# Kernel optimization log

Measured on AMD Instinct MI355X. Metric: run time of the kernel, lower is better.

## Reference

```python
import jax, jax.numpy as jnp
import numpy as np

TOKENS = 32768
D_MODEL = 4096
N_EXPERTS = 64
BALANCE_LOSS_WEIGHT = 0.1


def setup_inputs() -> dict:
    key = jax.random.key(0)
    kx, kw1, kw2, kn = jax.random.split(key, 4)
    x = jax.random.normal(kx, (TOKENS, D_MODEL), dtype=jnp.float32)
    # torch nn.Linear weight layout: [out_features, in_features]
    w1 = jax.random.normal(kw1, (N_EXPERTS, D_MODEL), dtype=jnp.float32) / np.sqrt(D_MODEL)
    w2 = jax.random.normal(kw2, (N_EXPERTS, N_EXPERTS), dtype=jnp.float32) / np.sqrt(N_EXPERTS)
    # fixed Gumbel noise sample: g = -log(-log(u)), matching gumbel_rsample
    u = jax.random.uniform(kn, (TOKENS, N_EXPERTS), dtype=jnp.float32, minval=1e-8, maxval=1.0)
    noise = -jnp.log(-jnp.log(u))
    return {"x": x, "w1": w1, "w2": w2, "noise": noise}


def reference(x, w1, w2, noise):
    # MLP gate: Linear(d->E, no bias) -> tanh -> Linear(E->E, no bias)
    h = jnp.tanh(x @ w1.T)                       # [T, E]
    logits = h @ w2.T                             # [T, E]
    scores = jax.nn.softmax(logits, axis=1)       # [T, E]
    logits_w_noise = logits + noise               # gumbel-perturbed logits
    top1_indices = jnp.argmax(logits_w_noise, axis=1)   # [T] int
    top1_scores = jnp.max(logits_w_noise, axis=1)       # [T]
    # balance loss
    importance_mean = scores.mean(axis=0)                        # [E]
    load = jnp.bincount(top1_indices, length=N_EXPERTS)          # [E] int
    load_mean = load.astype(scores.dtype) / x.shape[0]           # [E]
    balance_loss = (N_EXPERTS * jnp.sum(importance_mean * load_mean)
                    * BALANCE_LOSS_WEIGHT)
    return (top1_indices, top1_scores, balance_loss, load_mean, importance_mean)
```

## Files before the change

kernel.cpp:

```cpp
#include <hip/hip_runtime.h>
#include <math.h>

#define TOKENS 32768
#define DM 4096
#define NE 64
#define BALW 0.1f

#define TG 64
#define GBLOCKS (TOKENS / TG)

typedef __attribute__((ext_vector_type(8))) short short8;
typedef __attribute__((ext_vector_type(4))) float f32x4;

typedef unsigned short us;

__device__ inline us bf16r(float f) {
  const unsigned u = __float_as_uint(f);
  return (us)((u + 0x7FFFu + ((u >> 16) & 1u)) >> 16);
}
__device__ inline float bf16f(us s) {
  return __uint_as_float(((unsigned)s) << 16);
}
__device__ inline void split8(const float4 v0, const float4 v1, short8& H,
                              short8& M, short8& L) {
  float v[8] = {v0.x, v0.y, v0.z, v0.w, v1.x, v1.y, v1.z, v1.w};
#pragma unroll
  for (int j = 0; j < 8; ++j) {
    const us hs = bf16r(v[j]);
    const float r1 = v[j] - bf16f(hs);
    const us ms = bf16r(r1);
    const float r2 = r1 - bf16f(ms);
    const us ls = bf16r(r2);
    H[j] = (short)hs; M[j] = (short)ms; L[j] = (short)ls;
  }
}

__device__ inline void split8t(const float4 v0, const float4 v1, short8& H,
                               short8& M, short8& L) {
  unsigned u[8], um[8], ul[8];
  const float v[8] = {v0.x, v0.y, v0.z, v0.w, v1.x, v1.y, v1.z, v1.w};
#pragma unroll
  for (int j = 0; j < 8; ++j) {
    u[j] = __float_as_uint(v[j]);
    const float r1 = v[j] - __uint_as_float(u[j] & 0xFFFF0000u);
    um[j] = __float_as_uint(r1);
    const float r2 = r1 - __uint_as_float(um[j] & 0xFFFF0000u);
    ul[j] = __float_as_uint(r2);
  }
  union Cvt { unsigned u4[4]; short8 s8; } h, m, l;
#pragma unroll
  for (int d = 0; d < 4; ++d) {
    h.u4[d] = __builtin_amdgcn_perm(u[2 * d + 1], u[2 * d], 0x07060302u);
    m.u4[d] = __builtin_amdgcn_perm(um[2 * d + 1], um[2 * d], 0x07060302u);
    l.u4[d] = __builtin_amdgcn_perm(ul[2 * d + 1], ul[2 * d], 0x07060302u);
  }
  H = h.s8; M = m.s8; L = l.s8;
}

#define MFMA(a, b, c) __builtin_amdgcn_mfma_f32_16x16x32_bf16(a, b, c, 0, 0, 0)

__global__ void prep_w1_kernel(const float* __restrict__ w1,
                               us* __restrict__ bws) {
  const int kc = blockIdx.x;
  const int tid = threadIdx.x;
  const int ns = tid >> 6;
  const int l = tid & 63;
  const int r = l & 15, g = l >> 4;
  const int n = 16 * ns + r;
  const int kb = 32 * kc + 8 * g;
  const float* src = &w1[(size_t)n * DM + kb];
  const float4 v0 = *reinterpret_cast<const float4*>(src);
  const float4 v1 = *reinterpret_cast<const float4*>(src + 4);
  short8 H, M, L;
  split8(v0, v1, H, M, L);
  us* dst = bws + ((size_t)(kc * 4 + ns) * 3) * 512 + l * 8;
  *reinterpret_cast<short8*>(dst) = H;
  *reinterpret_cast<short8*>(dst + 512) = M;
  *reinterpret_cast<short8*>(dst + 1024) = L;
}

#define TMM 128

template <int SK>
__global__ __launch_bounds__(256, 2) void gemm_mfma_kernel(
    const float* __restrict__ x, const us* __restrict__ bws,
    float* __restrict__ hp) {
  constexpr int KS = DM / SK;
  constexpr int NIT = KS / 32;
  const int tid = threadIdx.x;
  const int kz = blockIdx.x % SK;
  const int mb = blockIdx.x / SK;
  const int w = tid >> 6;
  const int l = tid & 63;
  const int r = l & 15, g = l >> 4;
  const int row0 = mb * TMM + w * 32;
  const int kb0 = kz * KS;

  f32x4 acc[2][4];
#pragma unroll
  for (int i = 0; i < 2; ++i)
#pragma unroll
    for (int j = 0; j < 4; ++j) acc[i][j] = (f32x4)(0.f);

  const float* xA0 = &x[(size_t)(row0 + r) * DM + kb0 + 8 * g];
  const float* xA1 = xA0 + (size_t)16 * DM;
  const us* bb = bws + (size_t)(kb0 / 32) * 12 * 512 + l * 8;

  float4 a00 = *reinterpret_cast<const float4*>(xA0);
  float4 a01 = *reinterpret_cast<const float4*>(xA0 + 4);
  float4 a10 = *reinterpret_cast<const float4*>(xA1);
  float4 a11 = *reinterpret_cast<const float4*>(xA1 + 4);
  short8 bf[4][3];
#pragma unroll
  for (int ns = 0; ns < 4; ++ns)
#pragma unroll
    for (int p = 0; p < 3; ++p)
      bf[ns][p] = *reinterpret_cast<const short8*>(bb + (ns * 3 + p) * 512);

  for (int it = 0; it < NIT; ++it) {
    const int itn = (it + 1 < NIT) ? it + 1 : it;
    const us* btn = bb + (size_t)itn * 12 * 512;
    const int ko = itn * 32;
    const float4 n00 = *reinterpret_cast<const float4*>(xA0 + ko);
    const float4 n01 = *reinterpret_cast<const float4*>(xA0 + ko + 4);
    const float4 n10 = *reinterpret_cast<const float4*>(xA1 + ko);
    const float4 n11 = *reinterpret_cast<const float4*>(xA1 + ko + 4);

    short8 ah0, am0, al0, ah1, am1, al1;
    split8t(a00, a01, ah0, am0, al0);
    split8t(a10, a11, ah1, am1, al1);

#define PROW(AH0, AH1, P)                                                \
  do {                                                                   \
    _Pragma("unroll") for (int ns = 0; ns < 4; ++ns) {                   \
      acc[0][ns] = MFMA(AH0, bf[ns][P], acc[0][ns]);                     \
      acc[1][ns] = MFMA(AH1, bf[ns][P], acc[1][ns]);                     \
    }                                                                    \
  } while (0)
#define RELOAD(P)                                                        \
  do {                                                                   \
    _Pragma("unroll") for (int ns = 0; ns < 4; ++ns) bf[ns][P] =         \
        *reinterpret_cast<const short8*>(btn + (ns * 3 + (P)) * 512);    \
  } while (0)

    PROW(ah0, ah1, 0);
    PROW(am0, am1, 0);
    PROW(al0, al1, 0);
    RELOAD(0);
    PROW(ah0, ah1, 1);
    PROW(am0, am1, 1);
    RELOAD(1);
    PROW(ah0, ah1, 2);
    RELOAD(2);
#undef PROW
#undef RELOAD

    a00 = n00; a01 = n01; a10 = n10; a11 = n11;
  }

  float* dst = hp + (size_t)kz * TOKENS * NE;
#pragma unroll
  for (int ms = 0; ms < 2; ++ms)
#pragma unroll
    for (int ns = 0; ns < 4; ++ns)
#pragma unroll
      for (int q = 0; q < 4; ++q)
        dst[(size_t)(row0 + 16 * ms + 4 * g + q) * NE + 16 * ns + r] =
            acc[ms][ns][q];
}

#define TM 128
#define BK 32
#define LDSA 132
#define LDSB 68

template <int SK>
__global__ __launch_bounds__(256, 4) void gemm_fp32_kernel(
    const float* __restrict__ x, const float* __restrict__ w1,
    float* __restrict__ hp) {
  constexpr int KS = DM / SK;
  __shared__ float As[BK * LDSA];
  __shared__ float Ws[BK * LDSB];
  const int tid = threadIdx.x;
  const int kz = blockIdx.x % SK;
  const int mb = blockIdx.x / SK;
  const int row0 = mb * TM;
  const int kbase = kz * KS;
  const int m0 = (tid >> 3) * 4;
  const int n0 = (tid & 7) * 8;
  const int rS = tid >> 2;
  const int kS = (tid & 3) * 4;

  float acc[4][8];
#pragma unroll
  for (int i = 0; i < 4; ++i)
#pragma unroll
    for (int j = 0; j < 8; ++j) acc[i][j] = 0.f;

  float4 ra[4], rw[2];
  const float* xp = &x[(size_t)(row0 + rS) * DM + kS];
  const float* wp = &w1[(size_t)rS * DM + kS];

#define LOAD_TILE(KC)                                                   \
  do {                                                                  \
    ra[0] = *reinterpret_cast<const float4*>(xp + (KC));                \
    ra[1] = *reinterpret_cast<const float4*>(xp + (KC) + 16);           \
    ra[2] = *reinterpret_cast<const float4*>(xp + (size_t)64 * DM + (KC));\
    ra[3] = *reinterpret_cast<const float4*>(xp + (size_t)64 * DM + (KC) + 16);\
    rw[0] = *reinterpret_cast<const float4*>(wp + (KC));                \
    rw[1] = *reinterpret_cast<const float4*>(wp + (KC) + 16);           \
  } while (0)

#define ST4(arr, stride, krow, col, v)                                  \
  do {                                                                  \
    arr[((krow) + 0) * (stride) + (col)] = (v).x;                       \
    arr[((krow) + 1) * (stride) + (col)] = (v).y;                       \
    arr[((krow) + 2) * (stride) + (col)] = (v).z;                       \
    arr[((krow) + 3) * (stride) + (col)] = (v).w;                       \
  } while (0)

#define STORE_TILE()                                                    \
  do {                                                                  \
    ST4(As, LDSA, kS, rS, ra[0]);                                       \
    ST4(As, LDSA, kS + 16, rS, ra[1]);                                  \
    ST4(As, LDSA, kS, rS + 64, ra[2]);                                  \
    ST4(As, LDSA, kS + 16, rS + 64, ra[3]);                             \
    ST4(Ws, LDSB, kS, rS, rw[0]);                                       \
    ST4(Ws, LDSB, kS + 16, rS, rw[1]);                                  \
  } while (0)

  LOAD_TILE(kbase);

  for (int kc = kbase; kc < kbase + KS; kc += BK) {
    __syncthreads();
    STORE_TILE();
    __syncthreads();
    if (kc + BK < kbase + KS) LOAD_TILE(kc + BK);
#pragma unroll 8
    for (int k = 0; k < BK; ++k) {
      const float4 a0 = *reinterpret_cast<const float4*>(&As[k * LDSA + m0]);
      const float4 b0 = *reinterpret_cast<const float4*>(&Ws[k * LDSB + n0]);
      const float4 b1 =
          *reinterpret_cast<const float4*>(&Ws[k * LDSB + n0 + 4]);
      const float a[4] = {a0.x, a0.y, a0.z, a0.w};
      const float b[8] = {b0.x, b0.y, b0.z, b0.w, b1.x, b1.y, b1.z, b1.w};
#pragma unroll
      for (int i = 0; i < 4; ++i)
#pragma unroll
        for (int j = 0; j < 8; ++j) acc[i][j] = fmaf(a[i], b[j], acc[i][j]);
    }
  }
#undef LOAD_TILE
#undef ST4
#undef STORE_TILE

  float* dst = hp + (size_t)kz * TOKENS * NE;
#pragma unroll
  for (int i = 0; i < 4; ++i) {
    const size_t o = (size_t)(row0 + m0 + i) * NE;
    *reinterpret_cast<float4*>(&dst[o + n0]) =
        make_float4(acc[i][0], acc[i][1], acc[i][2], acc[i][3]);
    *reinterpret_cast<float4*>(&dst[o + n0 + 4]) =
        make_float4(acc[i][4], acc[i][5], acc[i][6], acc[i][7]);
  }
}

template <int SK>
__global__ __launch_bounds__(256) void gate_kernel(
    const float* __restrict__ hp, const float* __restrict__ w2,
    const float* __restrict__ noise, float* __restrict__ out_idx,
    float* __restrict__ out_score, float* __restrict__ imp_part,
    float* __restrict__ load_part) {
  __shared__ float hs[TG * 65];
  __shared__ float w2s[NE * 65];
  __shared__ float ls[TG * 66];
  __shared__ float csum[2 * NE];
  __shared__ int hist[NE];
  const int tid = threadIdx.x;
  const int t0 = blockIdx.x * TG;
  if (tid < NE) hist[tid] = 0;

#pragma unroll
  for (int it = 0; it < 4; ++it) {
    const int f = tid + 256 * it;
    const int c = f & 15;
    const int t = f >> 4;
    const size_t g = (size_t)(t0 + t) * NE + c * 4;
    float4 p = *reinterpret_cast<const float4*>(&hp[g]);
#pragma unroll
    for (int s = 1; s < SK; ++s) {
      const float4 q =
          *reinterpret_cast<const float4*>(&hp[(size_t)s * TOKENS * NE + g]);
      p.x += q.x; p.y += q.y; p.z += q.z; p.w += q.w;
    }
    float* d = &hs[t * 65 + c * 4];
    d[0] = tanhf(p.x);
    d[1] = tanhf(p.y);
    d[2] = tanhf(p.z);
    d[3] = tanhf(p.w);
  }
#pragma unroll
  for (int it = 0; it < 4; ++it) {
    const int f = tid + 256 * it;
    const int c = f & 15;
    const int rr = f >> 4;
    const float4 v =
        *reinterpret_cast<const float4*>(&w2[(size_t)rr * NE + c * 4]);
    float* d = &w2s[rr * 65 + c * 4];
    d[0] = v.x; d[1] = v.y; d[2] = v.z; d[3] = v.w;
  }
  __syncthreads();

  {
    const int m0 = (tid >> 4) * 4;
    const int n0 = (tid & 15) * 4;
    float acc[4][4];
#pragma unroll
    for (int i = 0; i < 4; ++i)
#pragma unroll
      for (int j = 0; j < 4; ++j) acc[i][j] = 0.f;
#pragma unroll 8
    for (int k = 0; k < NE; ++k) {
      float a[4], b[4];
#pragma unroll
      for (int i = 0; i < 4; ++i) a[i] = hs[(m0 + i) * 65 + k];
#pragma unroll
      for (int j = 0; j < 4; ++j) b[j] = w2s[(n0 + j) * 65 + k];
#pragma unroll
      for (int i = 0; i < 4; ++i)
#pragma unroll
        for (int j = 0; j < 4; ++j) acc[i][j] = fmaf(a[i], b[j], acc[i][j]);
    }
#pragma unroll
    for (int i = 0; i < 4; ++i)
#pragma unroll
      for (int j = 0; j < 4; ++j) ls[(m0 + i) * 66 + n0 + j] = acc[i][j];
  }
  __syncthreads();

  if (tid < TG) {
    const int t = tid;
    float mx = -INFINITY, best = -INFINITY;
    int bi = 0;
    for (int e = 0; e < NE; ++e) {
      const float lv = ls[t * 66 + e];
      mx = fmaxf(mx, lv);
      const float gg = lv + noise[(size_t)(t0 + t) * NE + e];
      if (gg > best) { best = gg; bi = e; }
    }
    float s = 0.f;
    for (int e = 0; e < NE; ++e) {
      const float ex = expf(ls[t * 66 + e] - mx);
      s += ex;
      ls[t * 66 + e] = ex;
    }
    const float inv = 1.f / s;
    for (int e = 0; e < NE; ++e) ls[t * 66 + e] *= inv;
    out_idx[t0 + t] = (float)bi;
    out_score[t0 + t] = best;
    atomicAdd(&hist[bi], 1);
  }
  __syncthreads();

  if (tid < 128) {
    const int e = tid & 63;
    const int half = tid >> 6;
    float s = 0.f;
    for (int rr = half * 32; rr < half * 32 + 32; ++rr) s += ls[rr * 66 + e];
    csum[half * NE + e] = s;
  }
  __syncthreads();
  if (tid < NE) {
    imp_part[(size_t)blockIdx.x * NE + tid] = csum[tid] + csum[NE + tid];
    load_part[(size_t)blockIdx.x * NE + tid] = (float)hist[tid];
  }
}

__global__ void finalize_kernel(const float* __restrict__ imp_part,
                                const float* __restrict__ load_part,
                                float* __restrict__ out) {
  const int e = threadIdx.x;
  float imp = 0.f, ld = 0.f;
  for (int b = 0; b < GBLOCKS; ++b) {
    imp += imp_part[(size_t)b * NE + e];
    ld += load_part[(size_t)b * NE + e];
  }
  const float imp_mean = imp / (float)TOKENS;
  const float load_mean = ld / (float)TOKENS;
  out[2 * TOKENS + 1 + e] = load_mean;
  out[2 * TOKENS + 1 + NE + e] = imp_mean;
  float prod = imp_mean * load_mean;
#pragma unroll
  for (int off = 32; off > 0; off >>= 1) prod += __shfl_down(prod, off);
  if (e == 0) out[2 * TOKENS] = (float)NE * prod * BALW;
}

extern "C" void kernel_launch(void* const* d_in, const int* in_sizes, int n_in,
                              void* d_out, int out_size, void* d_ws,
                              size_t ws_size, hipStream_t stream) {
  const float* x = (const float*)d_in[0];
  const float* w1 = (const float*)d_in[1];
  const float* w2 = (const float*)d_in[2];
  const float* noise = (const float*)d_in[3];
  float* out = (float*)d_out;

  const size_t bws_shorts = (size_t)128 * 4 * 3 * 512;
  const size_t part_elems = (size_t)2 * GBLOCKS * NE;
  const size_t need_mfma = bws_shorts * sizeof(us) +
                           ((size_t)2 * TOKENS * NE + part_elems) *
                               sizeof(float);
  const size_t need_fp32 =
      ((size_t)2 * TOKENS * NE + part_elems) * sizeof(float);

  if (ws_size == 0 || ws_size >= need_mfma) {
    us* bws = (us*)d_ws;
    float* hp = (float*)(bws + bws_shorts);
    float* imp_part = hp + (size_t)2 * TOKENS * NE;
    float* load_part = imp_part + (size_t)GBLOCKS * NE;
    hipLaunchKernelGGL(prep_w1_kernel, dim3(128), dim3(256), 0, stream, w1,
                       bws);
    hipLaunchKernelGGL((gemm_mfma_kernel<2>), dim3((TOKENS / TMM) * 2),
                       dim3(256), 0, stream, x, bws, hp);
    hipLaunchKernelGGL((gate_kernel<2>), dim3(GBLOCKS), dim3(256), 0, stream,
                       hp, w2, noise, out, out + TOKENS, imp_part, load_part);
    hipLaunchKernelGGL(finalize_kernel, dim3(1), dim3(64), 0, stream, imp_part,
                       load_part, out);
  } else if (ws_size >= need_fp32) {
    float* hp = (float*)d_ws;
    float* imp_part = hp + (size_t)2 * TOKENS * NE;
    float* load_part = imp_part + (size_t)GBLOCKS * NE;
    hipLaunchKernelGGL((gemm_fp32_kernel<2>), dim3((TOKENS / TM) * 2),
                       dim3(256), 0, stream, x, w1, hp);
    hipLaunchKernelGGL((gate_kernel<2>), dim3(GBLOCKS), dim3(256), 0, stream,
                       hp, w2, noise, out, out + TOKENS, imp_part, load_part);
    hipLaunchKernelGGL(finalize_kernel, dim3(1), dim3(64), 0, stream, imp_part,
                       load_part, out);
  }
}
```

Before: 202.3 us.

## Stage x tiles through LDS with coalesced loads; parallelize finalize reduction

The MFMA GEMM now loads 128x128 chunks of x with fully coalesced row-contiguous float4 loads into registers and writes them to shared memory. The next chunk is prefetched while the current one is consumed from LDS by the MFMA waves. Before, each lane read 32-byte pieces straight from global memory with a strided pattern. The finalize kernel now uses 1024 threads, splitting the per-block partial reduction into 16 segments combined through shared memory instead of one 64-thread serial loop. The cost is extra LDS traffic, two barriers per chunk, and much higher register use for the 16 staged float4s.

After: 313.6 us. 55.0% more time.

```diff
diff --git a/kernel.cpp b/kernel.cpp
--- a/kernel.cpp
+++ b/kernel.cpp
@@ -79,21 +79,24 @@
   *reinterpret_cast<short8*>(dst + 1024) = L;
 }
 
-#define TMM 128
+#define TMB 128
+#define KO 128
 
 template <int SK>
 __global__ __launch_bounds__(256, 2) void gemm_mfma_kernel(
     const float* __restrict__ x, const us* __restrict__ bws,
     float* __restrict__ hp) {
   constexpr int KS = DM / SK;
-  constexpr int NIT = KS / 32;
+  constexpr int NOUT = KS / KO;
+  constexpr int NCH = KS / 32;
+  __shared__ float As[TMB * 132];
   const int tid = threadIdx.x;
   const int kz = blockIdx.x % SK;
   const int mb = blockIdx.x / SK;
   const int w = tid >> 6;
   const int l = tid & 63;
   const int r = l & 15, g = l >> 4;
-  const int row0 = mb * TMM + w * 32;
+  const int row0 = mb * TMB;
   const int kb0 = kz * KS;
 
   f32x4 acc[2][4];
@@ -102,14 +105,15 @@
 #pragma unroll
     for (int j = 0; j < 4; ++j) acc[i][j] = (f32x4)(0.f);
 
-  const float* xA0 = &x[(size_t)(row0 + r) * DM + kb0 + 8 * g];
-  const float* xA1 = xA0 + (size_t)16 * DM;
+  const float* xstage =
+      &x[(size_t)(row0 + (tid >> 5)) * DM + kb0 + (tid & 31) * 4];
+  const int lds_w = (8 * 0 + (tid >> 5)) * 132 + (tid & 31) * 4;
+  float4 sa[16];
+#pragma unroll
+  for (int q = 0; q < 16; ++q)
+    sa[q] = *reinterpret_cast<const float4*>(xstage + (size_t)(8 * q) * DM);
+
   const us* bb = bws + (size_t)(kb0 / 32) * 12 * 512 + l * 8;
-
-  float4 a00 = *reinterpret_cast<const float4*>(xA0);
-  float4 a01 = *reinterpret_cast<const float4*>(xA0 + 4);
-  float4 a10 = *reinterpret_cast<const float4*>(xA1);
-  float4 a11 = *reinterpret_cast<const float4*>(xA1 + 4);
   short8 bf[4][3];
 #pragma unroll
   for (int ns = 0; ns < 4; ++ns)
@@ -117,20 +121,41 @@
     for (int p = 0; p < 3; ++p)
       bf[ns][p] = *reinterpret_cast<const short8*>(bb + (ns * 3 + p) * 512);
 
-  for (int it = 0; it < NIT; ++it) {
-    const int itn = (it + 1 < NIT) ? it + 1 : it;
-    const us* btn = bb + (size_t)itn * 12 * 512;
-    const int ko = itn * 32;
-    const float4 n00 = *reinterpret_cast<const float4*>(xA0 + ko);
-    const float4 n01 = *reinterpret_cast<const float4*>(xA0 + ko + 4);
-    const float4 n10 = *reinterpret_cast<const float4*>(xA1 + ko);
-    const float4 n11 = *reinterpret_cast<const float4*>(xA1 + ko + 4);
-
-    short8 ah0, am0, al0, ah1, am1, al1;
-    split8t(a00, a01, ah0, am0, al0);
-    split8t(a10, a11, ah1, am1, al1);
-
-#define PROW(AH0, AH1, P)                                                \
+  const int rbase = 32 * w + r;
+
+  for (int o = 0; o < NOUT; ++o) {
+    __syncthreads();
+#pragma unroll
+    for (int q = 0; q < 16; ++q)
+      *reinterpret_cast<float4*>(&As[lds_w + q * 8 * 132]) = sa[q];
+    __syncthreads();
+    if (o + 1 < NOUT) {
+#pragma unroll
+      for (int q = 0; q < 16; ++q)
+        sa[q] = *reinterpret_cast<const float4*>(
+            xstage + (size_t)(8 * q) * DM + (o + 1) * KO);
+    }
+
+#pragma unroll
+    for (int c = 0; c < 4; ++c) {
+      const int ic = o * 4 + c;
+      const int icn = (ic + 1 < NCH) ? ic + 1 : ic;
+      const us* btn = bb + (size_t)icn * 12 * 512;
+      const int ca = 32 * c + 8 * g;
+      const float4 a00 =
+          *reinterpret_cast<const float4*>(&As[rbase * 132 + ca]);
+      const float4 a01 =
+          *reinterpret_cast<const float4*>(&As[rbase * 132 + ca + 4]);
+      const float4 a10 =
+          *reinterpret_cast<const float4*>(&As[(rbase + 16) * 132 + ca]);
+      const float4 a11 =
+          *reinterpret_cast<const float4*>(&As[(rbase + 16) * 132 + ca + 4]);
+
+      short8 ah0, am0, al0, ah1, am1, al1;
+      split8t(a00, a01, ah0, am0, al0);
+      split8t(a10, a11, ah1, am1, al1);
+
+#define PROW2(AH0, AH1, P)                                               \
   do {                                                                   \
     _Pragma("unroll") for (int ns = 0; ns < 4; ++ns) {                   \
       acc[0][ns] = MFMA(AH0, bf[ns][P], acc[0][ns]);                     \
@@ -143,30 +168,29 @@
         *reinterpret_cast<const short8*>(btn + (ns * 3 + (P)) * 512);    \
   } while (0)
 
-    PROW(ah0, ah1, 0);
-    PROW(am0, am1, 0);
-    PROW(al0, al1, 0);
-    RELOAD(0);
-    PROW(ah0, ah1, 1);
-    PROW(am0, am1, 1);
-    RELOAD(1);
-    PROW(ah0, ah1, 2);
-    RELOAD(2);
-#undef PROW
+      PROW2(ah0, ah1, 0);
+      PROW2(am0, am1, 0);
+      PROW2(al0, al1, 0);
+      RELOAD(0);
+      PROW2(ah0, ah1, 1);
+      PROW2(am0, am1, 1);
+      RELOAD(1);
+      PROW2(ah0, ah1, 2);
+      RELOAD(2);
+#undef PROW2
 #undef RELOAD
-
-    a00 = n00; a01 = n01; a10 = n10; a11 = n11;
+    }
   }
 
   float* dst = hp + (size_t)kz * TOKENS * NE;
 #pragma unroll
-  for (int ms = 0; ms < 2; ++ms)
+  for (int rg = 0; rg < 2; ++rg)
 #pragma unroll
     for (int ns = 0; ns < 4; ++ns)
 #pragma unroll
       for (int q = 0; q < 4; ++q)
-        dst[(size_t)(row0 + 16 * ms + 4 * g + q) * NE + 16 * ns + r] =
-            acc[ms][ns][q];
+        dst[(size_t)(row0 + 32 * w + 16 * rg + 4 * g + q) * NE + 16 * ns +
+            r] = acc[rg][ns][q];
 }
 
 #define TM 128
@@ -379,20 +403,32 @@
 __global__ void finalize_kernel(const float* __restrict__ imp_part,
                                 const float* __restrict__ load_part,
                                 float* __restrict__ out) {
-  const int e = threadIdx.x;
+  __shared__ float si[16][NE];
+  __shared__ float sl[16][NE];
+  const int tid = threadIdx.x;
+  const int e = tid & 63;
+  const int seg = tid >> 6;
   float imp = 0.f, ld = 0.f;
-  for (int b = 0; b < GBLOCKS; ++b) {
+  for (int b = seg; b < GBLOCKS; b += 16) {
     imp += imp_part[(size_t)b * NE + e];
     ld += load_part[(size_t)b * NE + e];
   }
-  const float imp_mean = imp / (float)TOKENS;
-  const float load_mean = ld / (float)TOKENS;
-  out[2 * TOKENS + 1 + e] = load_mean;
-  out[2 * TOKENS + 1 + NE + e] = imp_mean;
-  float prod = imp_mean * load_mean;
-#pragma unroll
-  for (int off = 32; off > 0; off >>= 1) prod += __shfl_down(prod, off);
-  if (e == 0) out[2 * TOKENS] = (float)NE * prod * BALW;
+  si[seg][e] = imp;
+  sl[seg][e] = ld;
+  __syncthreads();
+  if (tid < NE) {
+    float ti = 0.f, tl = 0.f;
+#pragma unroll
+    for (int s = 0; s < 16; ++s) { ti += si[s][tid]; tl += sl[s][tid]; }
+    const float imp_mean = ti / (float)TOKENS;
+    const float load_mean = tl / (float)TOKENS;
+    out[2 * TOKENS + 1 + tid] = load_mean;
+    out[2 * TOKENS + 1 + NE + tid] = imp_mean;
+    float prod = imp_mean * load_mean;
+#pragma unroll
+    for (int off = 32; off > 0; off >>= 1) prod += __shfl_down(prod, off);
+    if (tid == 0) out[2 * TOKENS] = (float)NE * prod * BALW;
+  }
 }
 
 extern "C" void kernel_launch(void* const* d_in, const int* in_sizes, int n_in,
@@ -419,12 +455,12 @@
     float* load_part = imp_part + (size_t)GBLOCKS * NE;
     hipLaunchKernelGGL(prep_w1_kernel, dim3(128), dim3(256), 0, stream, w1,
                        bws);
-    hipLaunchKernelGGL((gemm_mfma_kernel<2>), dim3((TOKENS / TMM) * 2),
+    hipLaunchKernelGGL((gemm_mfma_kernel<2>), dim3((TOKENS / TMB) * 2),
                        dim3(256), 0, stream, x, bws, hp);
     hipLaunchKernelGGL((gate_kernel<2>), dim3(GBLOCKS), dim3(256), 0, stream,
                        hp, w2, noise, out, out + TOKENS, imp_part, load_part);
-    hipLaunchKernelGGL(finalize_kernel, dim3(1), dim3(64), 0, stream, imp_part,
-                       load_part, out);
+    hipLaunchKernelGGL(finalize_kernel, dim3(1), dim3(1024), 0, stream,
+                       imp_part, load_part, out);
   } else if (ws_size >= need_fp32) {
     float* hp = (float*)d_ws;
     float* imp_part = hp + (size_t)2 * TOKENS * NE;
@@ -433,7 +469,7 @@
                        dim3(256), 0, stream, x, w1, hp);
     hipLaunchKernelGGL((gate_kernel<2>), dim3(GBLOCKS), dim3(256), 0, stream,
                        hp, w2, noise, out, out + TOKENS, imp_part, load_part);
-    hipLaunchKernelGGL(finalize_kernel, dim3(1), dim3(64), 0, stream, imp_part,
-                       load_part, out);
-  }
-}
+    hipLaunchKernelGGL(finalize_kernel, dim3(1), dim3(1024), 0, stream,
+                       imp_part, load_part, out);
+  }
+}
```

## Use 512-thread MFMA blocks with 16 rows per wave and parallelize finalize

Applied to the files above, without the earlier changes.

The split-bf16 MFMA GEMM now gives each wave 16 rows instead of 32, with eight waves per 512-thread block. Fewer accumulators and fewer in-flight x loads per wave should cut register pressure and allow more waves per CU to hide memory latency. The trade-off is that each B fragment loaded from global memory now feeds half as many MFMAs, so B traffic per row doubles. The single-wave finalize kernel now uses 1024 threads, each striding over block partials, and combines them through shared memory, shortening its serial 512-iteration loop. The split8t helper is also reorganized to work pairwise, which mainly lowers register lifetime.

Result: slower. 261.8 us (+29.4%).

```diff
diff --git a/kernel.cpp b/kernel.cpp
--- a/kernel.cpp
+++ b/kernel.cpp
@@ -37,22 +37,22 @@
 
 __device__ inline void split8t(const float4 v0, const float4 v1, short8& H,
                                short8& M, short8& L) {
-  unsigned u[8], um[8], ul[8];
   const float v[8] = {v0.x, v0.y, v0.z, v0.w, v1.x, v1.y, v1.z, v1.w};
-#pragma unroll
-  for (int j = 0; j < 8; ++j) {
-    u[j] = __float_as_uint(v[j]);
-    const float r1 = v[j] - __uint_as_float(u[j] & 0xFFFF0000u);
-    um[j] = __float_as_uint(r1);
-    const float r2 = r1 - __uint_as_float(um[j] & 0xFFFF0000u);
-    ul[j] = __float_as_uint(r2);
-  }
   union Cvt { unsigned u4[4]; short8 s8; } h, m, l;
 #pragma unroll
   for (int d = 0; d < 4; ++d) {
-    h.u4[d] = __builtin_amdgcn_perm(u[2 * d + 1], u[2 * d], 0x07060302u);
-    m.u4[d] = __builtin_amdgcn_perm(um[2 * d + 1], um[2 * d], 0x07060302u);
-    l.u4[d] = __builtin_amdgcn_perm(ul[2 * d + 1], ul[2 * d], 0x07060302u);
+    const unsigned ua = __float_as_uint(v[2 * d]);
+    const unsigned ub = __float_as_uint(v[2 * d + 1]);
+    const float r1a = v[2 * d] - __uint_as_float(ua & 0xFFFF0000u);
+    const float r1b = v[2 * d + 1] - __uint_as_float(ub & 0xFFFF0000u);
+    const unsigned uma = __float_as_uint(r1a);
+    const unsigned umb = __float_as_uint(r1b);
+    const float r2a = r1a - __uint_as_float(uma & 0xFFFF0000u);
+    const float r2b = r1b - __uint_as_float(umb & 0xFFFF0000u);
+    h.u4[d] = __builtin_amdgcn_perm(ub, ua, 0x07060302u);
+    m.u4[d] = __builtin_amdgcn_perm(umb, uma, 0x07060302u);
+    l.u4[d] = __builtin_amdgcn_perm(__float_as_uint(r2b),
+                                    __float_as_uint(r2a), 0x07060302u);
   }
   H = h.s8; M = m.s8; L = l.s8;
 }
@@ -79,10 +79,8 @@
   *reinterpret_cast<short8*>(dst + 1024) = L;
 }
 
-#define TMM 128
-
 template <int SK>
-__global__ __launch_bounds__(256, 2) void gemm_mfma_kernel(
+__global__ __launch_bounds__(512, 4) void gemm_mfma_kernel(
     const float* __restrict__ x, const us* __restrict__ bws,
     float* __restrict__ hp) {
   constexpr int KS = DM / SK;
@@ -93,23 +91,18 @@
   const int w = tid >> 6;
   const int l = tid & 63;
   const int r = l & 15, g = l >> 4;
-  const int row0 = mb * TMM + w * 32;
+  const int wrow = mb * 128 + w * 16;
   const int kb0 = kz * KS;
 
-  f32x4 acc[2][4];
-#pragma unroll
-  for (int i = 0; i < 2; ++i)
-#pragma unroll
-    for (int j = 0; j < 4; ++j) acc[i][j] = (f32x4)(0.f);
-
-  const float* xA0 = &x[(size_t)(row0 + r) * DM + kb0 + 8 * g];
-  const float* xA1 = xA0 + (size_t)16 * DM;
+  f32x4 acc[4];
+#pragma unroll
+  for (int j = 0; j < 4; ++j) acc[j] = (f32x4)(0.f);
+
+  const float* xA = &x[(size_t)(wrow + r) * DM + kb0 + 8 * g];
   const us* bb = bws + (size_t)(kb0 / 32) * 12 * 512 + l * 8;
 
-  float4 a00 = *reinterpret_cast<const float4*>(xA0);
-  float4 a01 = *reinterpret_cast<const float4*>(xA0 + 4);
-  float4 a10 = *reinterpret_cast<const float4*>(xA1);
-  float4 a11 = *reinterpret_cast<const float4*>(xA1 + 4);
+  float4 a0 = *reinterpret_cast<const float4*>(xA);
+  float4 a1 = *reinterpret_cast<const float4*>(xA + 4);
   short8 bf[4][3];
 #pragma unroll
   for (int ns = 0; ns < 4; ++ns)
@@ -121,21 +114,16 @@
     const int itn = (it + 1 < NIT) ? it + 1 : it;
     const us* btn = bb + (size_t)itn * 12 * 512;
     const int ko = itn * 32;
-    const float4 n00 = *reinterpret_cast<const float4*>(xA0 + ko);
-    const float4 n01 = *reinterpret_cast<const float4*>(xA0 + ko + 4);
-    const float4 n10 = *reinterpret_cast<const float4*>(xA1 + ko);
-    const float4 n11 = *reinterpret_cast<const float4*>(xA1 + ko + 4);
-
-    short8 ah0, am0, al0, ah1, am1, al1;
-    split8t(a00, a01, ah0, am0, al0);
-    split8t(a10, a11, ah1, am1, al1);
-
-#define PROW(AH0, AH1, P)                                                \
+    const float4 n0 = *reinterpret_cast<const float4*>(xA + ko);
+    const float4 n1 = *reinterpret_cast<const float4*>(xA + ko + 4);
+
+    short8 ah, am, al;
+    split8t(a0, a1, ah, am, al);
+
+#define PROW(AH, P)                                                      \
   do {                                                                   \
-    _Pragma("unroll") for (int ns = 0; ns < 4; ++ns) {                   \
-      acc[0][ns] = MFMA(AH0, bf[ns][P], acc[0][ns]);                     \
-      acc[1][ns] = MFMA(AH1, bf[ns][P], acc[1][ns]);                     \
-    }                                                                    \
+    _Pragma("unroll") for (int ns = 0; ns < 4; ++ns) acc[ns] =           \
+        MFMA(AH, bf[ns][P], acc[ns]);                                    \
   } while (0)
 #define RELOAD(P)                                                        \
   do {                                                                   \
@@ -143,30 +131,27 @@
         *reinterpret_cast<const short8*>(btn + (ns * 3 + (P)) * 512);    \
   } while (0)
 
-    PROW(ah0, ah1, 0);
-    PROW(am0, am1, 0);
-    PROW(al0, al1, 0);
+    PROW(ah, 0);
+    PROW(am, 0);
+    PROW(al, 0);
     RELOAD(0);
-    PROW(ah0, ah1, 1);
-    PROW(am0, am1, 1);
+    PROW(ah, 1);
+    PROW(am, 1);
     RELOAD(1);
-    PROW(ah0, ah1, 2);
+    PROW(ah, 2);
     RELOAD(2);
 #undef PROW
 #undef RELOAD
 
-    a00 = n00; a01 = n01; a10 = n10; a11 = n11;
+    a0 = n0; a1 = n1;
   }
 
   float* dst = hp + (size_t)kz * TOKENS * NE;
 #pragma unroll
-  for (int ms = 0; ms < 2; ++ms)
-#pragma unroll
-    for (int ns = 0; ns < 4; ++ns)
-#pragma unroll
-      for (int q = 0; q < 4; ++q)
-        dst[(size_t)(row0 + 16 * ms + 4 * g + q) * NE + 16 * ns + r] =
-            acc[ms][ns][q];
+  for (int ns = 0; ns < 4; ++ns)
+#pragma unroll
+    for (int q = 0; q < 4; ++q)
+      dst[(size_t)(wrow + 4 * g + q) * NE + 16 * ns + r] = acc[ns][q];
 }
 
 #define TM 128
@@ -379,20 +364,32 @@
 __global__ void finalize_kernel(const float* __restrict__ imp_part,
                                 const float* __restrict__ load_part,
                                 float* __restrict__ out) {
-  const int e = threadIdx.x;
+  __shared__ float si[16][NE];
+  __shared__ float sl[16][NE];
+  const int tid = threadIdx.x;
+  const int e = tid & 63;
+  const int seg = tid >> 6;
   float imp = 0.f, ld = 0.f;
-  for (int b = 0; b < GBLOCKS; ++b) {
+  for (int b = seg; b < GBLOCKS; b += 16) {
     imp += imp_part[(size_t)b * NE + e];
     ld += load_part[(size_t)b * NE + e];
   }
-  const float imp_mean = imp / (float)TOKENS;
-  const float load_mean = ld / (float)TOKENS;
-  out[2 * TOKENS + 1 + e] = load_mean;
-  out[2 * TOKENS + 1 + NE + e] = imp_mean;
-  float prod = imp_mean * load_mean;
-#pragma unroll
-  for (int off = 32; off > 0; off >>= 1) prod += __shfl_down(prod, off);
-  if (e == 0) out[2 * TOKENS] = (float)NE * prod * BALW;
+  si[seg][e] = imp;
+  sl[seg][e] = ld;
+  __syncthreads();
+  if (tid < NE) {
+    float ti = 0.f, tl = 0.f;
+#pragma unroll
+    for (int s = 0; s < 16; ++s) { ti += si[s][tid]; tl += sl[s][tid]; }
+    const float imp_mean = ti / (float)TOKENS;
+    const float load_mean = tl / (float)TOKENS;
+    out[2 * TOKENS + 1 + tid] = load_mean;
+    out[2 * TOKENS + 1 + NE + tid] = imp_mean;
+    float prod = imp_mean * load_mean;
+#pragma unroll
+    for (int off = 32; off > 0; off >>= 1) prod += __shfl_down(prod, off);
+    if (tid == 0) out[2 * TOKENS] = (float)NE * prod * BALW;
+  }
 }
 
 extern "C" void kernel_launch(void* const* d_in, const int* in_sizes, int n_in,
@@ -419,12 +416,12 @@
     float* load_part = imp_part + (size_t)GBLOCKS * NE;
     hipLaunchKernelGGL(prep_w1_kernel, dim3(128), dim3(256), 0, stream, w1,
                        bws);
-    hipLaunchKernelGGL((gemm_mfma_kernel<2>), dim3((TOKENS / TMM) * 2),
-                       dim3(256), 0, stream, x, bws, hp);
+    hipLaunchKernelGGL((gemm_mfma_kernel<2>), dim3((TOKENS / 128) * 2),
+                       dim3(512), 0, stream, x, bws, hp);
     hipLaunchKernelGGL((gate_kernel<2>), dim3(GBLOCKS), dim3(256), 0, stream,
                        hp, w2, noise, out, out + TOKENS, imp_part, load_part);
-    hipLaunchKernelGGL(finalize_kernel, dim3(1), dim3(64), 0, stream, imp_part,
-                       load_part, out);
+    hipLaunchKernelGGL(finalize_kernel, dim3(1), dim3(1024), 0, stream,
+                       imp_part, load_part, out);
   } else if (ws_size >= need_fp32) {
     float* hp = (float*)d_ws;
     float* imp_part = hp + (size_t)2 * TOKENS * NE;
@@ -433,7 +430,7 @@
                        dim3(256), 0, stream, x, w1, hp);
     hipLaunchKernelGGL((gate_kernel<2>), dim3(GBLOCKS), dim3(256), 0, stream,
                        hp, w2, noise, out, out + TOKENS, imp_part, load_part);
-    hipLaunchKernelGGL(finalize_kernel, dim3(1), dim3(64), 0, stream, imp_part,
-                       load_part, out);
-  }
-}
+    hipLaunchKernelGGL(finalize_kernel, dim3(1), dim3(1024), 0, stream,
+                       imp_part, load_part, out);
+  }
+}
```
